# Performance work log

Measured on AMD Instinct MI355X. Metric: run time of the kernel, lower is better.

Reference implementation:

```python
import jax, jax.numpy as jnp
import numpy as np

TEMPERATURE = 0.07
NUM_NEGATIVES = 128
B, C, H, W = 4, 256, 32, 32
N_TOTAL = B * H * W  # 4096


def setup_inputs() -> dict:
    key = jax.random.key(0)
    k1, k2, k3 = jax.random.split(key, 3)
    feat_q = jax.random.normal(k1, (B, C, H, W), dtype=jnp.float32)
    feat_k = jax.random.normal(k2, (B, C, H, W), dtype=jnp.float32)
    # uniform draws in [0, N_TOTAL-1): same distribution as indexing into the
    # length-(N-1) 'choices' array in the original per-i loop
    neg_indices = jax.random.randint(k3, (N_TOTAL, NUM_NEGATIVES), 0, N_TOTAL - 1, dtype=jnp.int64 if jax.config.jax_enable_x64 else jnp.int32)
    return {"feat_q": feat_q, "feat_k": feat_k, "neg_indices": neg_indices}


def reference(feat_q, feat_k, neg_indices):
    b, c, h, w = feat_q.shape
    n = b * h * w
    q = feat_q.reshape(b, c, -1)
    k = feat_k.reshape(b, c, -1)
    # F.normalize(dim=1), eps=1e-12
    q = q / jnp.maximum(jnp.linalg.norm(q, axis=1, keepdims=True), 1e-12)
    k = k / jnp.maximum(jnp.linalg.norm(k, axis=1, keepdims=True), 1e-12)
    q = q.transpose(0, 2, 1).reshape(-1, c)  # [N, C]
    k = k.transpose(0, 2, 1).reshape(-1, c)  # [N, C]
    l_pos = jnp.sum(q * k, axis=1, keepdims=True)  # [N, 1]
    # self-exclusion: choices = all_idx without i -> shift sampled idx >= i up by 1
    row = jnp.arange(n, dtype=neg_indices.dtype)[:, None]
    idx = neg_indices + (neg_indices >= row).astype(neg_indices.dtype)  # [N, K]
    k_neg = k[idx]  # [N, K, C] gather
    l_neg = jnp.einsum('nc,nkc->nk', q, k_neg)  # [N, K]
    logits = jnp.concatenate([l_pos, l_neg], axis=1) / TEMPERATURE  # [N, 1+K]
    # cross-entropy with label 0 for every row
    loss = jnp.mean(jax.nn.logsumexp(logits, axis=1) - logits[:, 0])
    return loss
```

## Files before the change

### kernel.cpp

```cpp
#include <hip/hip_runtime.h>
#include <hip/hip_bf16.h>

#define N_TOTAL 4096
#define C_DIM 256
#define K_NEG 128
#define HW 1024
#define TEMP_INV (1.0f / 0.07f)

typedef _Float16 h8 __attribute__((ext_vector_type(8)));
typedef _Float16 h2 __attribute__((ext_vector_type(2)));

__global__ __launch_bounds__(256) void norm_tr_kernel(
    const float* __restrict__ fq, const float* __restrict__ fk,
    _Float16* __restrict__ qh, _Float16* __restrict__ kh) {
  const int bid = blockIdx.x;
  const int tensor = bid >> 8;
  const int chunk = bid & 255;
  const int n0 = chunk * 16;
  const int b = n0 / HW, s0 = n0 % HW;
  const float* base = (tensor ? fk : fq) + (size_t)b * C_DIM * HW + s0;
  _Float16* out = tensor ? kh : qh;
  const float scale_extra = tensor ? 1.0f : TEMP_INV;

  const int t = threadIdx.x;
  __shared__ float tile[16][C_DIM + 1];
  __shared__ float red[16][17];
  __shared__ float sinv[16];

  {
    const int c = t;
    const float* src = base + (size_t)c * HW;
#pragma unroll
    for (int p = 0; p < 4; ++p) {
      const float4 v = *(const float4*)(src + p * 4);
      tile[p * 4 + 0][c] = v.x;
      tile[p * 4 + 1][c] = v.y;
      tile[p * 4 + 2][c] = v.z;
      tile[p * 4 + 3][c] = v.w;
    }
  }
  __syncthreads();

  {
    const int s = t & 15, cg = t >> 4;
    float acc = 0.f;
#pragma unroll
    for (int i = 0; i < 16; ++i) {
      float v = tile[s][cg * 16 + i];
      acc = fmaf(v, v, acc);
    }
    red[s][cg] = acc;
  }
  __syncthreads();
  if (t < 16) {
    float tot = 0.f;
#pragma unroll
    for (int g = 0; g < 16; ++g) tot += red[t][g];
    sinv[t] = scale_extra / fmaxf(sqrtf(tot), 1e-12f);
  }
  __syncthreads();

  {
    const int s = t & 15, c16 = t >> 4;
    const float inv = sinv[s];
    h8 o0, o1;
#pragma unroll
    for (int j = 0; j < 8; ++j) o0[j] = (_Float16)(tile[s][c16 * 16 + j] * inv);
#pragma unroll
    for (int j = 0; j < 8; ++j)
      o1[j] = (_Float16)(tile[s][c16 * 16 + 8 + j] * inv);
    h8* dst = (h8*)(out + (size_t)(n0 + s) * C_DIM + c16 * 16);
    dst[0] = o0;
    dst[1] = o1;
  }
}

__global__ __launch_bounds__(256) void nce_kernel(
    const _Float16* __restrict__ qh, const _Float16* __restrict__ kh,
    const int* __restrict__ neg, float* __restrict__ loss_buf) {
  const int n = blockIdx.x;
  const int t = threadIdx.x;
  const int lane = t & 63;
  const int w = t >> 6;
  const int sub = lane & 7;
  const int unit = w * 8 + (lane >> 3);

  __shared__ float sneg[K_NEG];
  __shared__ float s_lpos;

  int r[4];
#pragma unroll
  for (int j = 0; j < 4; ++j) {
    int x = neg[(size_t)n * K_NEG + j * 32 + unit];
    r[j] = x + (x >= n ? 1 : 0);
  }
  const h8* qrow = (const h8*)(qh + (size_t)n * C_DIM);
  h8 qv[4];
#pragma unroll
  for (int i = 0; i < 4; ++i) qv[i] = qrow[i * 8 + sub];
  h8 kp[4];
  if (unit == 0) {
    const h8* kr = (const h8*)(kh + (size_t)n * C_DIM);
#pragma unroll
    for (int i = 0; i < 4; ++i) kp[i] = kr[i * 8 + sub];
  }
  h8 kd[4][4];
#pragma unroll
  for (int j = 0; j < 4; ++j) {
    const h8* kr = (const h8*)(kh + (size_t)r[j] * C_DIM);
#pragma unroll
    for (int i = 0; i < 4; ++i) kd[j][i] = kr[i * 8 + sub];
  }
  __builtin_amdgcn_sched_barrier(0);

  union H { h8 v; h2 p[4]; };

#pragma unroll
  for (int j = 0; j < 4; ++j) {
    float a0 = 0.f, a1 = 0.f;
#pragma unroll
    for (int i = 0; i < 4; ++i) {
      H a; a.v = qv[i];
      H b; b.v = kd[j][i];
      a0 = __builtin_amdgcn_fdot2(b.p[0], a.p[0], a0, false);
      a1 = __builtin_amdgcn_fdot2(b.p[1], a.p[1], a1, false);
      a0 = __builtin_amdgcn_fdot2(b.p[2], a.p[2], a0, false);
      a1 = __builtin_amdgcn_fdot2(b.p[3], a.p[3], a1, false);
    }
    float acc = a0 + a1;
    acc += __shfl_xor(acc, 1);
    acc += __shfl_xor(acc, 2);
    acc += __shfl_xor(acc, 4);
    if (sub == 0) sneg[j * 32 + unit] = acc;
  }
  if (unit == 0) {
    float a0 = 0.f, a1 = 0.f;
#pragma unroll
    for (int i = 0; i < 4; ++i) {
      H a; a.v = qv[i];
      H b; b.v = kp[i];
      a0 = __builtin_amdgcn_fdot2(b.p[0], a.p[0], a0, false);
      a1 = __builtin_amdgcn_fdot2(b.p[1], a.p[1], a1, false);
      a0 = __builtin_amdgcn_fdot2(b.p[2], a.p[2], a0, false);
      a1 = __builtin_amdgcn_fdot2(b.p[3], a.p[3], a1, false);
    }
    float acc = a0 + a1;
    acc += __shfl_xor(acc, 1);
    acc += __shfl_xor(acc, 2);
    acc += __shfl_xor(acc, 4);
    if (sub == 0) s_lpos = acc;
  }
  __syncthreads();

  if (w == 0) {
    float lp = s_lpos;
    float x1 = sneg[lane];
    float x2 = sneg[lane + 64];
    float m = fmaxf(fmaxf(x1, x2), lp);
#pragma unroll
    for (int off = 32; off; off >>= 1) m = fmaxf(m, __shfl_xor(m, off));
    float s = __expf(x1 - m) + __expf(x2 - m);
#pragma unroll
    for (int off = 32; off; off >>= 1) s += __shfl_xor(s, off);
    if (lane == 0) loss_buf[n] = m + __logf(s) - lp;
  }
}

__global__ __launch_bounds__(1024) void reduce_kernel(
    const float* __restrict__ loss_buf, float* __restrict__ out) {
  const int t = threadIdx.x;
  const float4 v = ((const float4*)loss_buf)[t];
  float s = (v.x + v.y) + (v.z + v.w);
#pragma unroll
  for (int off = 32; off; off >>= 1) s += __shfl_xor(s, off);
  __shared__ float red[16];
  if ((t & 63) == 0) red[t >> 6] = s;
  __syncthreads();
  if (t < 16) {
    float x = red[t];
#pragma unroll
    for (int off = 8; off; off >>= 1) x += __shfl_xor(x, off);
    if (t == 0) out[0] = x * (1.0f / N_TOTAL);
  }
}

extern "C" void kernel_launch(void* const* d_in, const int* in_sizes, int n_in,
                              void* d_out, int out_size, void* d_ws,
                              size_t ws_size, hipStream_t stream) {
  const float* fq = (const float*)d_in[0];
  const float* fk = (const float*)d_in[1];
  const int* neg = (const int*)d_in[2];
  float* out = (float*)d_out;

  _Float16* qh = (_Float16*)d_ws;
  _Float16* kh = qh + (size_t)N_TOTAL * C_DIM;
  float* loss_buf = (float*)(kh + (size_t)N_TOTAL * C_DIM);

  hipLaunchKernelGGL(norm_tr_kernel, dim3(512), dim3(256), 0, stream,
                     fq, fk, qh, kh);
  hipLaunchKernelGGL(nce_kernel, dim3(N_TOTAL), dim3(256), 0, stream,
                     qh, kh, neg, loss_buf);
  hipLaunchKernelGGL(reduce_kernel, dim3(1), dim3(1024), 0, stream,
                     loss_buf, out);
}
```

Measured before the change: 82.41 us.

## Process one row per wavefront and fuse final reduction via atomic last-block

```diff
diff --git a/kernel.cpp b/kernel.cpp
--- a/kernel.cpp
+++ b/kernel.cpp
@@ -12,7 +12,10 @@
 
 __global__ __launch_bounds__(256) void norm_tr_kernel(
     const float* __restrict__ fq, const float* __restrict__ fk,
-    _Float16* __restrict__ qh, _Float16* __restrict__ kh) {
+    _Float16* __restrict__ qh, _Float16* __restrict__ kh,
+    unsigned* __restrict__ counter) {
+  if (blockIdx.x == 0 && threadIdx.x == 0) *counter = 0u;
+
   const int bid = blockIdx.x;
   const int tensor = bid >> 8;
   const int chunk = bid & 255;
@@ -77,51 +80,38 @@
 
 __global__ __launch_bounds__(256) void nce_kernel(
     const _Float16* __restrict__ qh, const _Float16* __restrict__ kh,
-    const int* __restrict__ neg, float* __restrict__ loss_buf) {
-  const int n = blockIdx.x;
-  const int t = threadIdx.x;
-  const int lane = t & 63;
-  const int w = t >> 6;
+    const int* __restrict__ neg, float* __restrict__ loss_buf,
+    unsigned* __restrict__ counter, float* __restrict__ out) {
+  const int tid = threadIdx.x;
+  const int w = tid >> 6, lane = tid & 63;
   const int sub = lane & 7;
-  const int unit = w * 8 + (lane >> 3);
-
-  __shared__ float sneg[K_NEG];
-  __shared__ float s_lpos;
-
-  int r[4];
-#pragma unroll
-  for (int j = 0; j < 4; ++j) {
-    int x = neg[(size_t)n * K_NEG + j * 32 + unit];
-    r[j] = x + (x >= n ? 1 : 0);
-  }
+  const int unit = lane >> 3;
+  const int n = blockIdx.x * 4 + w;
+
+  union H { h8 v; h2 p[4]; };
+
   const h8* qrow = (const h8*)(qh + (size_t)n * C_DIM);
   h8 qv[4];
 #pragma unroll
   for (int i = 0; i < 4; ++i) qv[i] = qrow[i * 8 + sub];
+  const h8* kpr = (const h8*)(kh + (size_t)n * C_DIM);
   h8 kp[4];
-  if (unit == 0) {
-    const h8* kr = (const h8*)(kh + (size_t)n * C_DIM);
-#pragma unroll
-    for (int i = 0; i < 4; ++i) kp[i] = kr[i * 8 + sub];
-  }
-  h8 kd[4][4];
-#pragma unroll
-  for (int j = 0; j < 4; ++j) {
-    const h8* kr = (const h8*)(kh + (size_t)r[j] * C_DIM);
-#pragma unroll
-    for (int i = 0; i < 4; ++i) kd[j][i] = kr[i * 8 + sub];
-  }
-  __builtin_amdgcn_sched_barrier(0);
-
-  union H { h8 v; h2 p[4]; };
-
-#pragma unroll
-  for (int j = 0; j < 4; ++j) {
+#pragma unroll
+  for (int i = 0; i < 4; ++i) kp[i] = kpr[i * 8 + sub];
+
+  const int* nrow = neg + (size_t)n * K_NEG;
+  float x[16];
+
+#pragma unroll
+  for (int j = 0; j < 16; ++j) {
+    int idx = nrow[j * 8 + unit];
+    int r = idx + (idx >= n ? 1 : 0);
+    const h8* kr = (const h8*)(kh + (size_t)r * C_DIM);
     float a0 = 0.f, a1 = 0.f;
 #pragma unroll
     for (int i = 0; i < 4; ++i) {
       H a; a.v = qv[i];
-      H b; b.v = kd[j][i];
+      H b; b.v = kr[i * 8 + sub];
       a0 = __builtin_amdgcn_fdot2(b.p[0], a.p[0], a0, false);
       a1 = __builtin_amdgcn_fdot2(b.p[1], a.p[1], a1, false);
       a0 = __builtin_amdgcn_fdot2(b.p[2], a.p[2], a0, false);
@@ -131,9 +121,11 @@
     acc += __shfl_xor(acc, 1);
     acc += __shfl_xor(acc, 2);
     acc += __shfl_xor(acc, 4);
-    if (sub == 0) sneg[j * 32 + unit] = acc;
-  }
-  if (unit == 0) {
+    x[j] = acc;
+  }
+
+  float lp;
+  {
     float a0 = 0.f, a1 = 0.f;
 #pragma unroll
     for (int i = 0; i < 4; ++i) {
@@ -148,39 +140,44 @@
     acc += __shfl_xor(acc, 1);
     acc += __shfl_xor(acc, 2);
     acc += __shfl_xor(acc, 4);
-    if (sub == 0) s_lpos = acc;
-  }
-  __syncthreads();
-
-  if (w == 0) {
-    float lp = s_lpos;
-    float x1 = sneg[lane];
-    float x2 = sneg[lane + 64];
-    float m = fmaxf(fmaxf(x1, x2), lp);
-#pragma unroll
-    for (int off = 32; off; off >>= 1) m = fmaxf(m, __shfl_xor(m, off));
-    float s = __expf(x1 - m) + __expf(x2 - m);
-#pragma unroll
-    for (int off = 32; off; off >>= 1) s += __shfl_xor(s, off);
-    if (lane == 0) loss_buf[n] = m + __logf(s) - lp;
-  }
-}
-
-__global__ __launch_bounds__(1024) void reduce_kernel(
-    const float* __restrict__ loss_buf, float* __restrict__ out) {
-  const int t = threadIdx.x;
-  const float4 v = ((const float4*)loss_buf)[t];
-  float s = (v.x + v.y) + (v.z + v.w);
-#pragma unroll
-  for (int off = 32; off; off >>= 1) s += __shfl_xor(s, off);
-  __shared__ float red[16];
-  if ((t & 63) == 0) red[t >> 6] = s;
-  __syncthreads();
-  if (t < 16) {
-    float x = red[t];
-#pragma unroll
-    for (int off = 8; off; off >>= 1) x += __shfl_xor(x, off);
-    if (t == 0) out[0] = x * (1.0f / N_TOTAL);
+    lp = acc;
+  }
+
+  float m = x[0];
+#pragma unroll
+  for (int j = 1; j < 16; ++j) m = fmaxf(m, x[j]);
+  m = fmaxf(m, __shfl_xor(m, 8));
+  m = fmaxf(m, __shfl_xor(m, 16));
+  m = fmaxf(m, __shfl_xor(m, 32));
+  const float M = fmaxf(m, lp);
+  float s = 0.f;
+#pragma unroll
+  for (int j = 0; j < 16; ++j) s += __expf(x[j] - M);
+  s += __shfl_xor(s, 8);
+  s += __shfl_xor(s, 16);
+  s += __shfl_xor(s, 32);
+  const float total = s + __expf(lp - M);
+  if (lane == 0) loss_buf[n] = M + __logf(total) - lp;
+
+  __shared__ bool sdone;
+  __syncthreads();
+  if (tid == 0) {
+    __threadfence();
+    unsigned old = atomicAdd(counter, 1u);
+    sdone = (old == gridDim.x - 1);
+  }
+  __syncthreads();
+  if (sdone && w == 0) {
+    __threadfence();
+    float v = 0.f;
+#pragma unroll
+    for (int p = 0; p < 16; ++p) {
+      const float4 f = ((const float4*)loss_buf)[p * 64 + lane];
+      v += (f.x + f.y) + (f.z + f.w);
+    }
+#pragma unroll
+    for (int off = 32; off; off >>= 1) v += __shfl_xor(v, off);
+    if (lane == 0) out[0] = v * (1.0f / N_TOTAL);
   }
 }
 
@@ -195,11 +192,10 @@
   _Float16* qh = (_Float16*)d_ws;
   _Float16* kh = qh + (size_t)N_TOTAL * C_DIM;
   float* loss_buf = (float*)(kh + (size_t)N_TOTAL * C_DIM);
+  unsigned* counter = (unsigned*)(loss_buf + N_TOTAL);
 
   hipLaunchKernelGGL(norm_tr_kernel, dim3(512), dim3(256), 0, stream,
-                     fq, fk, qh, kh);
-  hipLaunchKernelGGL(nce_kernel, dim3(N_TOTAL), dim3(256), 0, stream,
-                     qh, kh, neg, loss_buf);
-  hipLaunchKernelGGL(reduce_kernel, dim3(1), dim3(1024), 0, stream,
-                     loss_buf, out);
+                     fq, fk, qh, kh, counter);
+  hipLaunchKernelGGL(nce_kernel, dim3(N_TOTAL / 4), dim3(256), 0, stream,
+                     qh, kh, neg, loss_buf, counter, out);
 }
```

Result: slower. 99.03 us (+20.2%).

## Map one wavefront per row with online softmax in NCE kernel

Applied to the files above, without the earlier changes.

```diff
diff --git a/kernel.cpp b/kernel.cpp
--- a/kernel.cpp
+++ b/kernel.cpp
@@ -28,15 +28,14 @@
   __shared__ float sinv[16];
 
   {
-    const int c = t;
-    const float* src = base + (size_t)c * HW;
+    const float* src = base + (size_t)t * HW;
 #pragma unroll
     for (int p = 0; p < 4; ++p) {
       const float4 v = *(const float4*)(src + p * 4);
-      tile[p * 4 + 0][c] = v.x;
-      tile[p * 4 + 1][c] = v.y;
-      tile[p * 4 + 2][c] = v.z;
-      tile[p * 4 + 3][c] = v.w;
+      tile[p * 4 + 0][t] = v.x;
+      tile[p * 4 + 1][t] = v.y;
+      tile[p * 4 + 2][t] = v.z;
+      tile[p * 4 + 3][t] = v.w;
     }
   }
   __syncthreads();
@@ -75,53 +74,39 @@
   }
 }
 
-__global__ __launch_bounds__(256) void nce_kernel(
+__global__ __launch_bounds__(512, 4) void nce_kernel(
     const _Float16* __restrict__ qh, const _Float16* __restrict__ kh,
     const int* __restrict__ neg, float* __restrict__ loss_buf) {
-  const int n = blockIdx.x;
-  const int t = threadIdx.x;
-  const int lane = t & 63;
-  const int w = t >> 6;
+  const int tid = threadIdx.x;
+  const int w = tid >> 6, lane = tid & 63;
   const int sub = lane & 7;
-  const int unit = w * 8 + (lane >> 3);
+  const int unit = lane >> 3;
+  const int n = blockIdx.x * 8 + w;
 
-  __shared__ float sneg[K_NEG];
-  __shared__ float s_lpos;
+  union H { h8 v; h2 p[4]; };
 
-  int r[4];
-#pragma unroll
-  for (int j = 0; j < 4; ++j) {
-    int x = neg[(size_t)n * K_NEG + j * 32 + unit];
-    r[j] = x + (x >= n ? 1 : 0);
-  }
   const h8* qrow = (const h8*)(qh + (size_t)n * C_DIM);
   h8 qv[4];
 #pragma unroll
   for (int i = 0; i < 4; ++i) qv[i] = qrow[i * 8 + sub];
+  const h8* kpr = (const h8*)(kh + (size_t)n * C_DIM);
   h8 kp[4];
-  if (unit == 0) {
-    const h8* kr = (const h8*)(kh + (size_t)n * C_DIM);
 #pragma unroll
-    for (int i = 0; i < 4; ++i) kp[i] = kr[i * 8 + sub];
-  }
-  h8 kd[4][4];
-#pragma unroll
-  for (int j = 0; j < 4; ++j) {
-    const h8* kr = (const h8*)(kh + (size_t)r[j] * C_DIM);
-#pragma unroll
-    for (int i = 0; i < 4; ++i) kd[j][i] = kr[i * 8 + sub];
-  }
-  __builtin_amdgcn_sched_barrier(0);
+  for (int i = 0; i < 4; ++i) kp[i] = kpr[i * 8 + sub];
 
-  union H { h8 v; h2 p[4]; };
+  const int* nrow = neg + (size_t)n * K_NEG + unit * 16;
 
-#pragma unroll
-  for (int j = 0; j < 4; ++j) {
+  float m = -1e30f, s = 0.f;
+#pragma unroll 2
+  for (int j = 0; j < 16; ++j) {
+    const int x = nrow[j];
+    const int r = x + (x >= n ? 1 : 0);
+    const h8* kr = (const h8*)(kh + (size_t)r * C_DIM);
     float a0 = 0.f, a1 = 0.f;
 #pragma unroll
     for (int i = 0; i < 4; ++i) {
       H a; a.v = qv[i];
-      H b; b.v = kd[j][i];
+      H b; b.v = kr[i * 8 + sub];
       a0 = __builtin_amdgcn_fdot2(b.p[0], a.p[0], a0, false);
       a1 = __builtin_amdgcn_fdot2(b.p[1], a.p[1], a1, false);
       a0 = __builtin_amdgcn_fdot2(b.p[2], a.p[2], a0, false);
@@ -131,9 +116,13 @@
     acc += __shfl_xor(acc, 1);
     acc += __shfl_xor(acc, 2);
     acc += __shfl_xor(acc, 4);
-    if (sub == 0) sneg[j * 32 + unit] = acc;
+    const float mn = fmaxf(m, acc);
+    s = s * __expf(m - mn) + __expf(acc - mn);
+    m = mn;
   }
-  if (unit == 0) {
+
+  float lp;
+  {
     float a0 = 0.f, a1 = 0.f;
 #pragma unroll
     for (int i = 0; i < 4; ++i) {
@@ -148,22 +137,20 @@
     acc += __shfl_xor(acc, 1);
     acc += __shfl_xor(acc, 2);
     acc += __shfl_xor(acc, 4);
-    if (sub == 0) s_lpos = acc;
+    lp = acc;
   }
-  __syncthreads();
 
-  if (w == 0) {
-    float lp = s_lpos;
-    float x1 = sneg[lane];
-    float x2 = sneg[lane + 64];
-    float m = fmaxf(fmaxf(x1, x2), lp);
 #pragma unroll
-    for (int off = 32; off; off >>= 1) m = fmaxf(m, __shfl_xor(m, off));
-    float s = __expf(x1 - m) + __expf(x2 - m);
-#pragma unroll
-    for (int off = 32; off; off >>= 1) s += __shfl_xor(s, off);
-    if (lane == 0) loss_buf[n] = m + __logf(s) - lp;
+  for (int off = 8; off <= 32; off <<= 1) {
+    const float mo = __shfl_xor(m, off);
+    const float so = __shfl_xor(s, off);
+    const float mn = fmaxf(m, mo);
+    s = s * __expf(m - mn) + so * __expf(mo - mn);
+    m = mn;
   }
+  const float M = fmaxf(m, lp);
+  const float stot = s * __expf(m - M) + __expf(lp - M);
+  if (lane == 0) loss_buf[n] = M + __logf(stot) - lp;
 }
 
 __global__ __launch_bounds__(1024) void reduce_kernel(
@@ -198,7 +185,7 @@
 
   hipLaunchKernelGGL(norm_tr_kernel, dim3(512), dim3(256), 0, stream,
                      fq, fk, qh, kh);
-  hipLaunchKernelGGL(nce_kernel, dim3(N_TOTAL), dim3(256), 0, stream,
+  hipLaunchKernelGGL(nce_kernel, dim3(N_TOTAL / 8), dim3(512), 0, stream,
                      qh, kh, neg, loss_buf);
   hipLaunchKernelGGL(reduce_kernel, dim3(1), dim3(1024), 0, stream,
                      loss_buf, out);
```

Result: no change. 80.99 us (-1.7%).
